# Kernel tuning notes

Measured on AMD Instinct MI355X. Metric: run time of the kernel, lower is better.

The kernel has to match this reference:

```python
import jax, jax.numpy as jnp
import numpy as np

S, B, C, H, M = 384, 8, 1024, 16, 1536
CC = C // H


def setup_inputs() -> dict:
    key = jax.random.key(0)
    ks = jax.random.split(key, 8)
    x = jax.random.normal(ks[0], (S, B, C), dtype=jnp.float32)
    pe = jax.random.normal(ks[1], (S, B, C), dtype=jnp.float32)
    memory_k = jax.random.normal(ks[2], (M, B, H, CC), dtype=jnp.float32)
    memory_v = jax.random.normal(ks[3], (M, B, H, CC), dtype=jnp.float32)
    w_qkv = jax.random.normal(ks[4], (C, 3 * C), dtype=jnp.float32) * 0.02
    b_qkv = jnp.zeros((3 * C,), dtype=jnp.float32)
    w_out = jax.random.normal(ks[5], (C, C), dtype=jnp.float32) * 0.02
    b_out = jnp.zeros((C,), dtype=jnp.float32)
    terminal = jnp.zeros((B,), dtype=bool)
    # causal mask over the new tokens: True = masked (future positions)
    content_mask = jnp.broadcast_to(
        (jnp.arange(S)[None, :] > jnp.arange(S)[:, None])[:, :, None], (S, S, B))
    padding_mask = jnp.zeros((S, B), dtype=bool)  # True = padded
    memory_length = jax.random.randint(ks[6], (B,), 0, M, dtype=jnp.int32)
    return dict(x=x, positional_encoding=pe, memory_k=memory_k, memory_v=memory_v,
                w_qkv=w_qkv, b_qkv=b_qkv, w_out=w_out, b_out=b_out,
                terminal=terminal, content_mask=content_mask,
                padding_mask=padding_mask, memory_length=memory_length)


def reference(x, positional_encoding, memory_k, memory_v, w_qkv, b_qkv,
              w_out, b_out, terminal, content_mask, padding_mask, memory_length):
    s, b, c = x.shape
    # qkv projection
    qkv = (x + positional_encoding) @ w_qkv + b_qkv          # [s,b,3c]
    q, k, v = jnp.split(qkv, 3, axis=-1)
    q = q.reshape(s, b, H, CC)
    k = k.reshape(s, b, H, CC)
    v = v.reshape(s, b, H, CC)
    # clear_memory(terminal): zero lengths for terminal episodes
    mem_len = jnp.where(terminal, 0, memory_length)          # [b]
    # ragged memory concat expressed with fixed capacity M + padding mask
    k_full = jnp.concatenate([memory_k, k], axis=0)          # [M+s,b,H,CC]
    v_full = jnp.concatenate([memory_v, v], axis=0)
    mem_pad = jnp.arange(M)[:, None] >= mem_len[None, :]     # [M,b] True=masked
    kv_pad = jnp.concatenate([mem_pad, padding_mask], axis=0)  # [M+s,b]
    mem_content = jnp.zeros((s, M, b), dtype=bool)           # memory visible to all queries
    full_content = jnp.concatenate([mem_content, content_mask], axis=1)  # [s,M+s,b]
    mask = full_content | kv_pad[None, :, :]                 # [s,M+s,b]
    # attention
    scores = jnp.einsum('sbhc,tbhc->stbh', q, k_full) * (1.0 / np.sqrt(CC))
    scores = jnp.where(mask[:, :, :, None], jnp.float32(-1e9), scores)
    p = jax.nn.softmax(scores, axis=1)                       # [s,M+s,b,h]
    out = jnp.einsum('stbh,tbhc->sbhc', p, v_full).reshape(s, b, c)
    return out @ w_out + b_out
```

## Files before the change

kernel.cpp:

```cpp
#include <hip/hip_runtime.h>
#include <math.h>

#define S_DIM 384
#define B_DIM 8
#define C_DIM 1024
#define H_DIM 16
#define M_DIM 1536
#define CC_DIM 64
#define ROWS  (S_DIM * B_DIM)
#define N3C   (3 * C_DIM)
#define NSPLIT 4

typedef unsigned short u16;
typedef short bf8v  __attribute__((ext_vector_type(8)));
typedef short bf4v  __attribute__((ext_vector_type(4)));
typedef u16   us8   __attribute__((ext_vector_type(8)));
typedef u16   us4   __attribute__((ext_vector_type(4)));
typedef float f4v   __attribute__((ext_vector_type(4)));

__device__ __forceinline__ u16 f2bf(float f) {
    unsigned u = __float_as_uint(f);
    u += 0x7fffu + ((u >> 16) & 1u);
    return (u16)(u >> 16);
}
__device__ __forceinline__ float bf2f(u16 v) {
    return __uint_as_float(((unsigned)v) << 16);
}
#if __has_builtin(__builtin_amdgcn_exp2f)
#define EX2(x) __builtin_amdgcn_exp2f(x)
#else
#define EX2(x) __expf((x) * 0.69314718056f)
#endif
#define QSCALE (0.125f * 1.44269504f)

__device__ __forceinline__ f4v mfma16x16x16bf16(bf4v a, bf4v b, f4v c) {
#if __has_builtin(__builtin_amdgcn_mfma_f32_16x16x16bf16_1k)
    return __builtin_amdgcn_mfma_f32_16x16x16bf16_1k(a, b, c, 0, 0, 0);
#else
    return c;
#endif
}

__device__ __forceinline__ void gload16(const u16* g, u16* l) {
    __builtin_amdgcn_global_load_lds(
        (const __attribute__((address_space(1))) void*)g,
        (__attribute__((address_space(3))) void*)l, 16, 0, 0);
}

__device__ __forceinline__ void tr32(const float* __restrict__ in, u16* __restrict__ out,
                                     int R, int Cc, int r0, int c0, int tid, float* sm) {
    #pragma unroll
    for (int i = 0; i < 4; i++) {
        int r = i * 8 + (tid >> 5), c = tid & 31;
        sm[r * 33 + c] = in[(size_t)(r0 + r) * Cc + c0 + c];
    }
    __syncthreads();
    #pragma unroll
    for (int i = 0; i < 4; i++) {
        int cw = i * 8 + (tid >> 5), rw = tid & 31;
        out[(size_t)(c0 + cw) * R + r0 + rw] = f2bf(sm[rw * 33 + cw]);
    }
}

__global__ __launch_bounds__(256) void prep_all(
    const float* __restrict__ x, const float* __restrict__ pe, u16* __restrict__ Abf,
    const float* __restrict__ wqkv, u16* __restrict__ Wqkvt,
    const float* __restrict__ wout, u16* __restrict__ Woutt,
    const float* __restrict__ mk, u16* __restrict__ mk_bf,
    const float* __restrict__ mv, u16* __restrict__ mv_t)
{
    __shared__ float sm[64 * 65];
    const int bid = blockIdx.x, tid = threadIdx.x;

    if (bid < 3072) {
        size_t i = ((size_t)bid * 256 + tid) * 4;
        float4 xv = *(const float4*)(x + i);
        float4 pv = *(const float4*)(pe + i);
        us4 o;
        o[0] = f2bf(xv.x + pv.x); o[1] = f2bf(xv.y + pv.y);
        o[2] = f2bf(xv.z + pv.z); o[3] = f2bf(xv.w + pv.w);
        *(us4*)(Abf + i) = o;
    } else if (bid < 6144) {
        int b2 = bid - 3072;
        tr32(wqkv, Wqkvt, C_DIM, N3C, (b2 / 96) * 32, (b2 % 96) * 32, tid, sm);
    } else if (bid < 7168) {
        int b3 = bid - 6144;
        tr32(wout, Woutt, C_DIM, C_DIM, (b3 / 32) * 32, (b3 % 32) * 32, tid, sm);
    } else if (bid < 19456) {
        int b4 = bid - 7168;
        size_t i = ((size_t)b4 * 256 + tid) * 4;
        float4 v = *(const float4*)(mk + i);
        us4 o;
        o[0] = f2bf(v.x); o[1] = f2bf(v.y); o[2] = f2bf(v.z); o[3] = f2bf(v.w);
        *(us4*)(mk_bf + i) = o;
    } else {
        int b5 = bid - 19456;
        int bh = b5 & 127;
        int t0 = (b5 >> 7) * 64;
        #pragma unroll
        for (int i = 0; i < 16; i++) {
            int r = i * 4 + (tid >> 6), c = tid & 63;
            sm[r * 65 + c] = mv[((size_t)(t0 + r) * 128 + bh) * 64 + c];
        }
        __syncthreads();
        #pragma unroll
        for (int i = 0; i < 16; i++) {
            int cc = i * 4 + (tid >> 6), tw = tid & 63;
            mv_t[((size_t)bh * 64 + cc) * M_DIM + t0 + tw] = f2bf(sm[tw * 65 + cc]);
        }
    }
}

__global__ __launch_bounds__(256) void prep_vwt(
    const u16* __restrict__ Vw, u16* __restrict__ Vwt)
{
    __shared__ u16 tile[64][66];
    const int tid = threadIdx.x;
    const int bh = blockIdx.x & 127;
    const int t0 = (blockIdx.x >> 7) * 64;
    #pragma unroll
    for (int i = 0; i < 16; i++) {
        int r = i * 4 + (tid >> 6), c = tid & 63;
        tile[r][c] = Vw[((size_t)bh * S_DIM + t0 + r) * 64 + c];
    }
    __syncthreads();
    #pragma unroll
    for (int i = 0; i < 16; i++) {
        int cc = i * 4 + (tid >> 6), tw = tid & 63;
        Vwt[((size_t)bh * 64 + cc) * S_DIM + t0 + tw] = tile[tw][cc];
    }
}

__global__ __launch_bounds__(256) void qkv_gemm(
    const u16* __restrict__ Abf, const u16* __restrict__ Wt,
    const float* __restrict__ bias,
    u16* __restrict__ Qw, u16* __restrict__ Kw, u16* __restrict__ Vw)
{
    __shared__ u16 smem[128 * 64 + 64 * 64];
    u16* As = smem;
    u16* Bs = smem + 128 * 64;
    u16* Cs = smem;

    const int tid = threadIdx.x;
    const int lane = tid & 63, w = tid >> 6;
    const int lr = lane & 15, quad = lane >> 4;
    const int wm = w >> 1, wn = w & 1;
    const int row0 = blockIdx.y * 128, col0 = blockIdx.x * 64;

    f4v acc[4][2];
    #pragma unroll
    for (int i = 0; i < 4; i++)
        #pragma unroll
        for (int j = 0; j < 2; j++)
            acc[i][j] = (f4v){0.f, 0.f, 0.f, 0.f};

    for (int k0 = 0; k0 < C_DIM; k0 += 64) {
        __syncthreads();
        #pragma unroll
        for (int j = 0; j < 4; j++) {
            int idx = j * 256 + tid;
            int r = idx >> 3, c = (idx & 7) ^ (r & 7);
            gload16(&Abf[(size_t)(row0 + r) * C_DIM + k0 + c * 8], &As[idx * 8]);
        }
        #pragma unroll
        for (int j = 0; j < 2; j++) {
            int idx = j * 256 + tid;
            int r = idx >> 3, c = (idx & 7) ^ (r & 7);
            gload16(&Wt[(size_t)(col0 + r) * C_DIM + k0 + c * 8], &Bs[idx * 8]);
        }
        __syncthreads();
        #pragma unroll
        for (int kh = 0; kh < 2; kh++) {
            bf8v a[4], b[2];
            #pragma unroll
            for (int mi = 0; mi < 4; mi++) {
                int row = wm * 64 + mi * 16 + lr;
                int p = (kh * 4 + quad) ^ (lr & 7);
                a[mi] = *(const bf8v*)&As[row * 64 + p * 8];
            }
            #pragma unroll
            for (int nj = 0; nj < 2; nj++) {
                int row = wn * 32 + nj * 16 + lr;
                int p = (kh * 4 + quad) ^ (lr & 7);
                b[nj] = *(const bf8v*)&Bs[row * 64 + p * 8];
            }
            #pragma unroll
            for (int mi = 0; mi < 4; mi++)
                #pragma unroll
                for (int nj = 0; nj < 2; nj++)
                    acc[mi][nj] = __builtin_amdgcn_mfma_f32_16x16x32_bf16(a[mi], b[nj], acc[mi][nj], 0, 0, 0);
        }
    }

    const int which = col0 >> 10;
    const int h = (col0 >> 6) & 15;
    const float qs = (which == 0) ? QSCALE : 1.0f;
    u16* dstbuf = (which == 0) ? Qw : ((which == 1) ? Kw : Vw);

    __syncthreads();
    #pragma unroll
    for (int nj = 0; nj < 2; nj++) {
        int col = col0 + wn * 32 + nj * 16 + lr;
        float bv = bias[col];
        #pragma unroll
        for (int mi = 0; mi < 4; mi++)
            #pragma unroll
            for (int reg = 0; reg < 4; reg++)
                Cs[(wm * 64 + mi * 16 + quad * 4 + reg) * 72 + wn * 32 + nj * 16 + lr] =
                    f2bf((acc[mi][nj][reg] + bv) * qs);
    }
    __syncthreads();
    {
        int r = tid >> 1, half = tid & 1;
        int rg = row0 + r, s = rg >> 3, bb = rg & 7;
        u16* drow = dstbuf + ((size_t)(bb * 16 + h) * S_DIM + s) * 64 + half * 32;
        #pragma unroll
        for (int i = 0; i < 4; i++)
            *(us8*)(drow + i * 8) = *(const us8*)&Cs[r * 72 + half * 32 + i * 8];
    }
}

__global__ __launch_bounds__(256) void attn_split(
    const u16* __restrict__ Qw, const u16* __restrict__ Kw,
    const u16* __restrict__ mk_bf, const u16* __restrict__ Vwt,
    const u16* __restrict__ mv_t, const unsigned char* __restrict__ terminal,
    const int* __restrict__ mem_len, u16* __restrict__ Op, float* __restrict__ ml)
{
    __shared__ u16 smem[2 * 64 * 64];
    u16* Ks = smem;
    u16* Vs = smem + 64 * 64;
    u16* Os = smem;

    const int tid = threadIdx.x;
    const int lane = tid & 63, w = tid >> 6;
    const int lr = lane & 15, quad = lane >> 4, q8 = quad * 8;
    const int bid = blockIdx.x;
    const int split = bid & (NSPLIT - 1);
    const int g = bid / NSPLIT;
    const int b = g & 7, h = (g >> 3) & 15, sc = g >> 7;
    const int bh = b * 16 + h, sq0 = sc * 64;
    const int L = terminal[b] ? 0 : mem_len[b];
    const int qrow = sq0 + w * 16 + lr;

    const u16* qbase = Qw + ((size_t)bh * S_DIM + sq0 + w * 16 + lr) * 64;
    bf8v qf0 = *(const bf8v*)&qbase[q8];
    bf8v qf1 = *(const bf8v*)&qbase[32 + q8];

    f4v O[4];
    #pragma unroll
    for (int nj = 0; nj < 4; nj++) O[nj] = (f4v){0.f, 0.f, 0.f, 0.f};
    float m_i = -1e30f, l_i = 0.0f;

    const int memChunks = (L + 63) >> 6;
    const int total = memChunks + sc + 1;
    const int lo = (split * total) / NSPLIT;
    const int hi = ((split + 1) * total) / NSPLIT;

    const f4v zero = (f4v){0.f, 0.f, 0.f, 0.f};

    for (int ch = lo; ch < hi; ch++) {
        const bool isMem = (ch < memChunks);
        const int tloc = isMem ? ch * 64 : (ch - memChunks) * 64;
        const u16* kb; size_t kstr;
        if (isMem) { kb = mk_bf + ((size_t)tloc * 128 + bh) * 64; kstr = 128 * 64; }
        else       { kb = Kw + ((size_t)bh * S_DIM + tloc) * 64; kstr = 64; }
        const u16* vb; size_t vstr;
        if (isMem) { vb = mv_t + (size_t)bh * 64 * M_DIM + tloc; vstr = M_DIM; }
        else       { vb = Vwt + (size_t)bh * 64 * S_DIM + tloc; vstr = S_DIM; }

        __syncthreads();
        #pragma unroll
        for (int j = 0; j < 2; j++) {
            int idx = j * 256 + tid;
            int r = idx >> 3, c = (idx & 7) ^ (r & 7);
            gload16(kb + (size_t)r * kstr + c * 8, &Ks[idx * 8]);
        }
        #pragma unroll
        for (int j = 0; j < 2; j++) {
            int idx = j * 256 + tid;
            int cc = idx >> 3, c = (idx & 7) ^ (cc & 7);
            gload16(vb + (size_t)cc * vstr + c * 8, &Vs[idx * 8]);
        }
        __syncthreads();

        f4v sv[4];
        #pragma unroll
        for (int tt = 0; tt < 4; tt++) {
            int row = tt * 16 + lr;
            int p0 = quad ^ (lr & 7), p1 = (4 + quad) ^ (lr & 7);
            bf8v k0 = *(const bf8v*)&Ks[row * 64 + p0 * 8];
            bf8v k1 = *(const bf8v*)&Ks[row * 64 + p1 * 8];
            sv[tt] = __builtin_amdgcn_mfma_f32_16x16x32_bf16(k0, qf0, zero, 0, 0, 0);
            sv[tt] = __builtin_amdgcn_mfma_f32_16x16x32_bf16(k1, qf1, sv[tt], 0, 0, 0);
        }

        if (isMem) {
            if (tloc + 64 > L) {
                #pragma unroll
                for (int tt = 0; tt < 4; tt++)
                    #pragma unroll
                    for (int reg = 0; reg < 4; reg++) {
                        int t = tloc + tt * 16 + quad * 4 + reg;
                        if (t >= L) sv[tt][reg] = -1e30f;
                    }
            }
        } else {
            if (tloc + 63 > sq0 + w * 16) {
                #pragma unroll
                for (int tt = 0; tt < 4; tt++)
                    #pragma unroll
                    for (int reg = 0; reg < 4; reg++) {
                        int t = tloc + tt * 16 + quad * 4 + reg;
                        if (t > qrow) sv[tt][reg] = -1e30f;
                    }
            }
        }

        float rowmax = fmaxf(fmaxf(sv[0][0], sv[0][1]), fmaxf(sv[0][2], sv[0][3]));
        #pragma unroll
        for (int tt = 1; tt < 4; tt++)
            rowmax = fmaxf(rowmax, fmaxf(fmaxf(sv[tt][0], sv[tt][1]),
                                         fmaxf(sv[tt][2], sv[tt][3])));
        rowmax = fmaxf(rowmax, __shfl_xor(rowmax, 16));
        rowmax = fmaxf(rowmax, __shfl_xor(rowmax, 32));
        float mnew = fmaxf(m_i, rowmax);
        float alpha = EX2(m_i - mnew);
        m_i = mnew;
        float sum = 0.0f;
        bf4v pf[4];
        #pragma unroll
        for (int tt = 0; tt < 4; tt++) {
            #pragma unroll
            for (int reg = 0; reg < 4; reg++) {
                float p = EX2(sv[tt][reg] - mnew);
                sum += p;
                pf[tt][reg] = (short)f2bf(p);
            }
        }
        sum += __shfl_xor(sum, 16);
        sum += __shfl_xor(sum, 32);
        l_i = l_i * alpha + sum;

        float alphaR[4];
        #pragma unroll
        for (int reg = 0; reg < 4; reg++)
            alphaR[reg] = __shfl(alpha, quad * 4 + reg);
        #pragma unroll
        for (int nj = 0; nj < 4; nj++)
            #pragma unroll
            for (int reg = 0; reg < 4; reg++)
                O[nj][reg] *= alphaR[reg];

        #pragma unroll
        for (int tt = 0; tt < 4; tt++) {
            #pragma unroll
            for (int nj = 0; nj < 4; nj++) {
                int cc = nj * 16 + lr;
                int c = (tt * 2 + (quad >> 1)) ^ (lr & 7);
                bf4v vf = *(const bf4v*)&Vs[cc * 64 + c * 8 + (quad & 1) * 4];
                O[nj] = mfma16x16x16bf16(pf[tt], vf, O[nj]);
            }
        }
    }

    const size_t pbase = (size_t)(g * NSPLIT + split) * 64;
    if (quad == 0) {
        int row = w * 16 + lr;
        float2 mlv = {m_i, l_i};
        *(float2*)&ml[(pbase + row) * 2] = mlv;
    }
    __syncthreads();
    #pragma unroll
    for (int reg = 0; reg < 4; reg++)
        #pragma unroll
        for (int nj = 0; nj < 4; nj++)
            Os[(w * 16 + quad * 4 + reg) * 72 + nj * 16 + lr] = f2bf(O[nj][reg]);
    __syncthreads();
    {
        int row = tid >> 2, q4 = tid & 3;
        us8 v0 = *(const us8*)&Os[row * 72 + q4 * 16];
        us8 v1 = *(const us8*)&Os[row * 72 + q4 * 16 + 8];
        size_t ob = (pbase + row) * 64 + q4 * 16;
        *(us8*)&Op[ob] = v0;
        *(us8*)&Op[ob + 8] = v1;
    }
}

__global__ __launch_bounds__(256) void attn_combine(
    const u16* __restrict__ Op, const float* __restrict__ ml, u16* __restrict__ Obf)
{
    const int g = blockIdx.x;
    const int b = g & 7, h = (g >> 3) & 15, sc = g >> 7;
    const int tid = threadIdx.x;
    const int row = tid >> 2, c0 = (tid & 3) * 16;

    float m[NSPLIT], lv[NSPLIT];
    #pragma unroll
    for (int j = 0; j < NSPLIT; j++) {
        size_t base = (size_t)(g * NSPLIT + j) * 64 + row;
        m[j]  = ml[base * 2];
        lv[j] = ml[base * 2 + 1];
    }
    float mstar = m[0];
    #pragma unroll
    for (int j = 1; j < NSPLIT; j++) mstar = fmaxf(mstar, m[j]);
    float sc_j[NSPLIT], l = 0.0f;
    #pragma unroll
    for (int j = 0; j < NSPLIT; j++) {
        sc_j[j] = EX2(m[j] - mstar);
        l += sc_j[j] * lv[j];
    }
    float inv = 1.0f / l;

    float o[16];
    #pragma unroll
    for (int c = 0; c < 16; c++) o[c] = 0.0f;
    #pragma unroll
    for (int j = 0; j < NSPLIT; j++) {
        const u16* src = &Op[((size_t)(g * NSPLIT + j) * 64 + row) * 64 + c0];
        us8 v0 = *(const us8*)src;
        us8 v1 = *(const us8*)(src + 8);
        #pragma unroll
        for (int c = 0; c < 8; c++) {
            o[c]     += sc_j[j] * bf2f(v0[c]);
            o[c + 8] += sc_j[j] * bf2f(v1[c]);
        }
    }
    int s = sc * 64 + row;
    size_t dst = ((size_t)s * 8 + b) * C_DIM + h * 64 + c0;
    us8 w0, w1;
    #pragma unroll
    for (int c = 0; c < 8; c++) {
        w0[c] = f2bf(o[c] * inv);
        w1[c] = f2bf(o[c + 8] * inv);
    }
    *(us8*)&Obf[dst] = w0;
    *(us8*)&Obf[dst + 8] = w1;
}

__global__ __launch_bounds__(256) void proj_gemm(
    const u16* __restrict__ Abf, const u16* __restrict__ Wt,
    const float* __restrict__ bias, float* __restrict__ out)
{
    __shared__ u16 As[128 * 64];
    __shared__ u16 Bs[64 * 64];
    const int tid = threadIdx.x;
    const int lane = tid & 63, w = tid >> 6;
    const int lr = lane & 15, quad = lane >> 4;
    const int wm = w >> 1, wn = w & 1;
    const int row0 = blockIdx.y * 128, col0 = blockIdx.x * 64;

    f4v acc[4][2];
    #pragma unroll
    for (int i = 0; i < 4; i++)
        #pragma unroll
        for (int j = 0; j < 2; j++)
            acc[i][j] = (f4v){0.f, 0.f, 0.f, 0.f};

    for (int k0 = 0; k0 < C_DIM; k0 += 64) {
        __syncthreads();
        #pragma unroll
        for (int j = 0; j < 4; j++) {
            int idx = j * 256 + tid;
            int r = idx >> 3, c = (idx & 7) ^ (r & 7);
            gload16(&Abf[(size_t)(row0 + r) * C_DIM + k0 + c * 8], &As[idx * 8]);
        }
        #pragma unroll
        for (int j = 0; j < 2; j++) {
            int idx = j * 256 + tid;
            int r = idx >> 3, c = (idx & 7) ^ (r & 7);
            gload16(&Wt[(size_t)(col0 + r) * C_DIM + k0 + c * 8], &Bs[idx * 8]);
        }
        __syncthreads();
        #pragma unroll
        for (int kh = 0; kh < 2; kh++) {
            bf8v a[4], b[2];
            #pragma unroll
            for (int mi = 0; mi < 4; mi++) {
                int row = wm * 64 + mi * 16 + lr;
                int p = (kh * 4 + quad) ^ (lr & 7);
                a[mi] = *(const bf8v*)&As[row * 64 + p * 8];
            }
            #pragma unroll
            for (int nj = 0; nj < 2; nj++) {
                int row = wn * 32 + nj * 16 + lr;
                int p = (kh * 4 + quad) ^ (lr & 7);
                b[nj] = *(const bf8v*)&Bs[row * 64 + p * 8];
            }
            #pragma unroll
            for (int mi = 0; mi < 4; mi++)
                #pragma unroll
                for (int nj = 0; nj < 2; nj++)
                    acc[mi][nj] = __builtin_amdgcn_mfma_f32_16x16x32_bf16(a[mi], b[nj], acc[mi][nj], 0, 0, 0);
        }
    }

    #pragma unroll
    for (int nj = 0; nj < 2; nj++) {
        int col = col0 + wn * 32 + nj * 16 + lr;
        float bv = bias[col];
        #pragma unroll
        for (int mi = 0; mi < 4; mi++) {
            #pragma unroll
            for (int reg = 0; reg < 4; reg++) {
                int rg = row0 + wm * 64 + mi * 16 + quad * 4 + reg;
                out[(size_t)rg * C_DIM + col] = acc[mi][nj][reg] + bv;
            }
        }
    }
}

extern "C" void kernel_launch(void* const* d_in, const int* in_sizes, int n_in,
                              void* d_out, int out_size, void* d_ws, size_t ws_size,
                              hipStream_t stream) {
    const float* x    = (const float*)d_in[0];
    const float* pe   = (const float*)d_in[1];
    const float* mk   = (const float*)d_in[2];
    const float* mv   = (const float*)d_in[3];
    const float* wqkv = (const float*)d_in[4];
    const float* bqkv = (const float*)d_in[5];
    const float* wout = (const float*)d_in[6];
    const float* bout = (const float*)d_in[7];
    const unsigned char* term = (const unsigned char*)d_in[8];
    const int* mem_len = (const int*)d_in[11];

    char* ws = (char*)d_ws;
    u16* Abf   = (u16*)(ws + 0);
    u16* Obf   = (u16*)(ws + 0);
    u16* Wqkvt = (u16*)(ws + 6291456);
    u16* Vwt   = (u16*)(ws + 6291456);
    u16* Woutt = (u16*)(ws + 12582912);
    u16* mk_bf = (u16*)(ws + 14680064);
    u16* mv_t  = (u16*)(ws + 39845888);
    u16* Qw    = (u16*)(ws + 65011712);
    u16* Kw    = (u16*)(ws + 71303168);
    u16* Vw    = (u16*)(ws + 77594624);
    u16* Op    = (u16*)(ws + 83886080);
    float* ml  = (float*)(ws + 109051904);

    float* out = (float*)d_out;

    prep_all<<<22528, 256, 0, stream>>>(x, pe, Abf, wqkv, Wqkvt, wout, Woutt,
                                        mk, mk_bf, mv, mv_t);

    qkv_gemm<<<dim3(N3C / 64, ROWS / 128), 256, 0, stream>>>(
        Abf, Wqkvt, bqkv, Qw, Kw, Vw);

    prep_vwt<<<(S_DIM / 64) * 128, 256, 0, stream>>>(Vw, Vwt);

    attn_split<<<B_DIM * H_DIM * (S_DIM / 64) * NSPLIT, 256, 0, stream>>>(
        Qw, Kw, mk_bf, Vwt, mv_t, term, mem_len, Op, ml);

    attn_combine<<<B_DIM * H_DIM * (S_DIM / 64), 256, 0, stream>>>(Op, ml, Obf);

    proj_gemm<<<dim3(C_DIM / 64, ROWS / 128), 256, 0, stream>>>(
        Obf, Woutt, bout, out);
}
```

Before: 303.2 us.

## Fuse V transpose into QKV GEMM, fixed-size attention splits, smaller proj tiles

Several changes land together. The QKV GEMM epilogue now writes V already transposed, so the separate prep_vwt kernel and its launch are removed. Attention splits the KV range into fixed 6-chunk pieces, up to 5 splits per query tile; blocks with no work exit early and the combine step reads only the splits that exist. The projection GEMM moves to 64x64 tiles for more blocks, the prep kernel handles two vectors per thread, and the attention output is written straight from registers instead of staged through LDS. The trade-offs are uncoalesced scalar Op stores and more partial buffers than before.

```diff
diff --git a/kernel.cpp b/kernel.cpp
--- a/kernel.cpp
+++ b/kernel.cpp
@@ -9,7 +9,8 @@
 #define CC_DIM 64
 #define ROWS  (S_DIM * B_DIM)
 #define N3C   (3 * C_DIM)
-#define NSPLIT 4
+#define CHUNK 6
+#define MAXS  5
 
 typedef unsigned short u16;
 typedef short bf8v  __attribute__((ext_vector_type(8)));
@@ -72,29 +73,36 @@
     __shared__ float sm[64 * 65];
     const int bid = blockIdx.x, tid = threadIdx.x;
 
-    if (bid < 3072) {
-        size_t i = ((size_t)bid * 256 + tid) * 4;
-        float4 xv = *(const float4*)(x + i);
-        float4 pv = *(const float4*)(pe + i);
-        us4 o;
-        o[0] = f2bf(xv.x + pv.x); o[1] = f2bf(xv.y + pv.y);
-        o[2] = f2bf(xv.z + pv.z); o[3] = f2bf(xv.w + pv.w);
-        *(us4*)(Abf + i) = o;
-    } else if (bid < 6144) {
-        int b2 = bid - 3072;
+    if (bid < 1536) {
+        size_t i0 = (size_t)bid * 2048 + tid * 4;
+        #pragma unroll
+        for (int j = 0; j < 2; j++) {
+            size_t i = i0 + j * 1024;
+            float4 xv = *(const float4*)(x + i);
+            float4 pv = *(const float4*)(pe + i);
+            us4 o;
+            o[0] = f2bf(xv.x + pv.x); o[1] = f2bf(xv.y + pv.y);
+            o[2] = f2bf(xv.z + pv.z); o[3] = f2bf(xv.w + pv.w);
+            *(us4*)(Abf + i) = o;
+        }
+    } else if (bid < 4608) {
+        int b2 = bid - 1536;
         tr32(wqkv, Wqkvt, C_DIM, N3C, (b2 / 96) * 32, (b2 % 96) * 32, tid, sm);
-    } else if (bid < 7168) {
-        int b3 = bid - 6144;
+    } else if (bid < 5632) {
+        int b3 = bid - 4608;
         tr32(wout, Woutt, C_DIM, C_DIM, (b3 / 32) * 32, (b3 % 32) * 32, tid, sm);
-    } else if (bid < 19456) {
-        int b4 = bid - 7168;
-        size_t i = ((size_t)b4 * 256 + tid) * 4;
-        float4 v = *(const float4*)(mk + i);
-        us4 o;
-        o[0] = f2bf(v.x); o[1] = f2bf(v.y); o[2] = f2bf(v.z); o[3] = f2bf(v.w);
-        *(us4*)(mk_bf + i) = o;
+    } else if (bid < 11776) {
+        size_t i0 = (size_t)(bid - 5632) * 2048 + tid * 4;
+        #pragma unroll
+        for (int j = 0; j < 2; j++) {
+            size_t i = i0 + j * 1024;
+            float4 v = *(const float4*)(mk + i);
+            us4 o;
+            o[0] = f2bf(v.x); o[1] = f2bf(v.y); o[2] = f2bf(v.z); o[3] = f2bf(v.w);
+            *(us4*)(mk_bf + i) = o;
+        }
     } else {
-        int b5 = bid - 19456;
+        int b5 = bid - 11776;
         int bh = b5 & 127;
         int t0 = (b5 >> 7) * 64;
         #pragma unroll
@@ -111,30 +119,10 @@
     }
 }
 
-__global__ __launch_bounds__(256) void prep_vwt(
-    const u16* __restrict__ Vw, u16* __restrict__ Vwt)
-{
-    __shared__ u16 tile[64][66];
-    const int tid = threadIdx.x;
-    const int bh = blockIdx.x & 127;
-    const int t0 = (blockIdx.x >> 7) * 64;
-    #pragma unroll
-    for (int i = 0; i < 16; i++) {
-        int r = i * 4 + (tid >> 6), c = tid & 63;
-        tile[r][c] = Vw[((size_t)bh * S_DIM + t0 + r) * 64 + c];
-    }
-    __syncthreads();
-    #pragma unroll
-    for (int i = 0; i < 16; i++) {
-        int cc = i * 4 + (tid >> 6), tw = tid & 63;
-        Vwt[((size_t)bh * 64 + cc) * S_DIM + t0 + tw] = tile[tw][cc];
-    }
-}
-
 __global__ __launch_bounds__(256) void qkv_gemm(
     const u16* __restrict__ Abf, const u16* __restrict__ Wt,
     const float* __restrict__ bias,
-    u16* __restrict__ Qw, u16* __restrict__ Kw, u16* __restrict__ Vw)
+    u16* __restrict__ Qw, u16* __restrict__ Kw, u16* __restrict__ Vwt)
 {
     __shared__ u16 smem[128 * 64 + 64 * 64];
     u16* As = smem;
@@ -195,7 +183,6 @@
     const int which = col0 >> 10;
     const int h = (col0 >> 6) & 15;
     const float qs = (which == 0) ? QSCALE : 1.0f;
-    u16* dstbuf = (which == 0) ? Qw : ((which == 1) ? Kw : Vw);
 
     __syncthreads();
     #pragma unroll
@@ -210,13 +197,31 @@
                     f2bf((acc[mi][nj][reg] + bv) * qs);
     }
     __syncthreads();
-    {
+
+    if (which != 2) {
+        u16* dstbuf = (which == 0) ? Qw : Kw;
         int r = tid >> 1, half = tid & 1;
         int rg = row0 + r, s = rg >> 3, bb = rg & 7;
         u16* drow = dstbuf + ((size_t)(bb * 16 + h) * S_DIM + s) * 64 + half * 32;
         #pragma unroll
         for (int i = 0; i < 4; i++)
             *(us8*)(drow + i * 8) = *(const us8*)&Cs[r * 72 + half * 32 + i * 8];
+    } else {
+        int cc = tid & 63, w4 = tid >> 6;
+        int s0 = row0 >> 3;
+        #pragma unroll
+        for (int pb = 0; pb < 2; pb++) {
+            int bb = w4 * 2 + pb;
+            us8 v0, v1;
+            #pragma unroll
+            for (int sl = 0; sl < 8; sl++) {
+                v0[sl] = Cs[(sl * 8 + bb) * 72 + cc];
+                v1[sl] = Cs[((sl + 8) * 8 + bb) * 72 + cc];
+            }
+            u16* dr = Vwt + ((size_t)(bb * 16 + h) * 64 + cc) * S_DIM + s0;
+            *(us8*)dr = v0;
+            *(us8*)(dr + 8) = v1;
+        }
     }
 }
 
@@ -226,20 +231,24 @@
     const u16* __restrict__ mv_t, const unsigned char* __restrict__ terminal,
     const int* __restrict__ mem_len, u16* __restrict__ Op, float* __restrict__ ml)
 {
-    __shared__ u16 smem[2 * 64 * 64];
-    u16* Ks = smem;
-    u16* Vs = smem + 64 * 64;
-    u16* Os = smem;
+    __shared__ u16 Ks[64 * 64];
+    __shared__ u16 Vs[64 * 64];
 
     const int tid = threadIdx.x;
     const int lane = tid & 63, w = tid >> 6;
     const int lr = lane & 15, quad = lane >> 4, q8 = quad * 8;
     const int bid = blockIdx.x;
-    const int split = bid & (NSPLIT - 1);
-    const int g = bid / NSPLIT;
+    const int j = bid % MAXS;
+    const int g = bid / MAXS;
     const int b = g & 7, h = (g >> 3) & 15, sc = g >> 7;
     const int bh = b * 16 + h, sq0 = sc * 64;
     const int L = terminal[b] ? 0 : mem_len[b];
+    const int memChunks = (L + 63) >> 6;
+    const int total = memChunks + sc + 1;
+    const int lo = j * CHUNK;
+    const int hi = (lo + CHUNK < total) ? lo + CHUNK : total;
+    if (lo >= total) return;
+
     const int qrow = sq0 + w * 16 + lr;
 
     const u16* qbase = Qw + ((size_t)bh * S_DIM + sq0 + w * 16 + lr) * 64;
@@ -250,11 +259,6 @@
     #pragma unroll
     for (int nj = 0; nj < 4; nj++) O[nj] = (f4v){0.f, 0.f, 0.f, 0.f};
     float m_i = -1e30f, l_i = 0.0f;
-
-    const int memChunks = (L + 63) >> 6;
-    const int total = memChunks + sc + 1;
-    const int lo = (split * total) / NSPLIT;
-    const int hi = ((split + 1) * total) / NSPLIT;
 
     const f4v zero = (f4v){0.f, 0.f, 0.f, 0.f};
 
@@ -270,14 +274,14 @@
 
         __syncthreads();
         #pragma unroll
-        for (int j = 0; j < 2; j++) {
-            int idx = j * 256 + tid;
+        for (int jj = 0; jj < 2; jj++) {
+            int idx = jj * 256 + tid;
             int r = idx >> 3, c = (idx & 7) ^ (r & 7);
             gload16(kb + (size_t)r * kstr + c * 8, &Ks[idx * 8]);
         }
         #pragma unroll
-        for (int j = 0; j < 2; j++) {
-            int idx = j * 256 + tid;
+        for (int jj = 0; jj < 2; jj++) {
+            int idx = jj * 256 + tid;
             int cc = idx >> 3, c = (idx & 7) ^ (cc & 7);
             gload16(vb + (size_t)cc * vstr + c * 8, &Vs[idx * 8]);
         }
@@ -363,30 +367,23 @@
         }
     }
 
-    const size_t pbase = (size_t)(g * NSPLIT + split) * 64;
+    const size_t pbase = (size_t)(g * MAXS + j) * 64;
     if (quad == 0) {
         int row = w * 16 + lr;
         float2 mlv = {m_i, l_i};
         *(float2*)&ml[(pbase + row) * 2] = mlv;
     }
-    __syncthreads();
-    #pragma unroll
-    for (int reg = 0; reg < 4; reg++)
+    #pragma unroll
+    for (int reg = 0; reg < 4; reg++) {
+        int row = w * 16 + quad * 4 + reg;
         #pragma unroll
         for (int nj = 0; nj < 4; nj++)
-            Os[(w * 16 + quad * 4 + reg) * 72 + nj * 16 + lr] = f2bf(O[nj][reg]);
-    __syncthreads();
-    {
-        int row = tid >> 2, q4 = tid & 3;
-        us8 v0 = *(const us8*)&Os[row * 72 + q4 * 16];
-        us8 v1 = *(const us8*)&Os[row * 72 + q4 * 16 + 8];
-        size_t ob = (pbase + row) * 64 + q4 * 16;
-        *(us8*)&Op[ob] = v0;
-        *(us8*)&Op[ob + 8] = v1;
+            Op[(pbase + row) * 64 + nj * 16 + lr] = f2bf(O[nj][reg]);
     }
 }
 
 __global__ __launch_bounds__(256) void attn_combine(
+    const unsigned char* __restrict__ terminal, const int* __restrict__ mem_len,
     const u16* __restrict__ Op, const float* __restrict__ ml, u16* __restrict__ Obf)
 {
     const int g = blockIdx.x;
@@ -394,20 +391,26 @@
     const int tid = threadIdx.x;
     const int row = tid >> 2, c0 = (tid & 3) * 16;
 
-    float m[NSPLIT], lv[NSPLIT];
-    #pragma unroll
-    for (int j = 0; j < NSPLIT; j++) {
-        size_t base = (size_t)(g * NSPLIT + j) * 64 + row;
-        m[j]  = ml[base * 2];
-        lv[j] = ml[base * 2 + 1];
+    const int L = terminal[b] ? 0 : mem_len[b];
+    const int total = ((L + 63) >> 6) + sc + 1;
+    const int nsp = (total + CHUNK - 1) / CHUNK;
+
+    float m[MAXS], lv[MAXS];
+    #pragma unroll
+    for (int j = 0; j < MAXS; j++) {
+        if (j < nsp) {
+            size_t base = (size_t)(g * MAXS + j) * 64 + row;
+            m[j]  = ml[base * 2];
+            lv[j] = ml[base * 2 + 1];
+        } else { m[j] = -1e30f; lv[j] = 0.0f; }
     }
     float mstar = m[0];
     #pragma unroll
-    for (int j = 1; j < NSPLIT; j++) mstar = fmaxf(mstar, m[j]);
-    float sc_j[NSPLIT], l = 0.0f;
-    #pragma unroll
-    for (int j = 0; j < NSPLIT; j++) {
-        sc_j[j] = EX2(m[j] - mstar);
+    for (int j = 1; j < MAXS; j++) mstar = fmaxf(mstar, m[j]);
+    float sc_j[MAXS], l = 0.0f;
+    #pragma unroll
+    for (int j = 0; j < MAXS; j++) {
+        sc_j[j] = (j < nsp) ? EX2(m[j] - mstar) : 0.0f;
         l += sc_j[j] * lv[j];
     }
     float inv = 1.0f / l;
@@ -415,9 +418,8 @@
     float o[16];
     #pragma unroll
     for (int c = 0; c < 16; c++) o[c] = 0.0f;
-    #pragma unroll
-    for (int j = 0; j < NSPLIT; j++) {
-        const u16* src = &Op[((size_t)(g * NSPLIT + j) * 64 + row) * 64 + c0];
+    for (int j = 0; j < nsp; j++) {
+        const u16* src = &Op[((size_t)(g * MAXS + j) * 64 + row) * 64 + c0];
         us8 v0 = *(const us8*)src;
         us8 v1 = *(const us8*)(src + 8);
         #pragma unroll
@@ -442,70 +444,47 @@
     const u16* __restrict__ Abf, const u16* __restrict__ Wt,
     const float* __restrict__ bias, float* __restrict__ out)
 {
-    __shared__ u16 As[128 * 64];
+    __shared__ u16 As[64 * 64];
     __shared__ u16 Bs[64 * 64];
     const int tid = threadIdx.x;
     const int lane = tid & 63, w = tid >> 6;
     const int lr = lane & 15, quad = lane >> 4;
-    const int wm = w >> 1, wn = w & 1;
-    const int row0 = blockIdx.y * 128, col0 = blockIdx.x * 64;
-
-    f4v acc[4][2];
-    #pragma unroll
-    for (int i = 0; i < 4; i++)
-        #pragma unroll
-        for (int j = 0; j < 2; j++)
-            acc[i][j] = (f4v){0.f, 0.f, 0.f, 0.f};
+    const int row0 = blockIdx.y * 64, col0 = blockIdx.x * 64;
+
+    f4v acc[4];
+    #pragma unroll
+    for (int i = 0; i < 4; i++) acc[i] = (f4v){0.f, 0.f, 0.f, 0.f};
 
     for (int k0 = 0; k0 < C_DIM; k0 += 64) {
         __syncthreads();
         #pragma unroll
-        for (int j = 0; j < 4; j++) {
+        for (int j = 0; j < 2; j++) {
             int idx = j * 256 + tid;
             int r = idx >> 3, c = (idx & 7) ^ (r & 7);
             gload16(&Abf[(size_t)(row0 + r) * C_DIM + k0 + c * 8], &As[idx * 8]);
-        }
-        #pragma unroll
-        for (int j = 0; j < 2; j++) {
-            int idx = j * 256 + tid;
-            int r = idx >> 3, c = (idx & 7) ^ (r & 7);
             gload16(&Wt[(size_t)(col0 + r) * C_DIM + k0 + c * 8], &Bs[idx * 8]);
         }
         __syncthreads();
         #pragma unroll
         for (int kh = 0; kh < 2; kh++) {
-            bf8v a[4], b[2];
-            #pragma unroll
-            for (int mi = 0; mi < 4; mi++) {
-                int row = wm * 64 + mi * 16 + lr;
-                int p = (kh * 4 + quad) ^ (lr & 7);
-                a[mi] = *(const bf8v*)&As[row * 64 + p * 8];
-            }
-            #pragma unroll
-            for (int nj = 0; nj < 2; nj++) {
-                int row = wn * 32 + nj * 16 + lr;
-                int p = (kh * 4 + quad) ^ (lr & 7);
-                b[nj] = *(const bf8v*)&Bs[row * 64 + p * 8];
-            }
-            #pragma unroll
-            for (int mi = 0; mi < 4; mi++)
-                #pragma unroll
-                for (int nj = 0; nj < 2; nj++)
-                    acc[mi][nj] = __builtin_amdgcn_mfma_f32_16x16x32_bf16(a[mi], b[nj], acc[mi][nj], 0, 0, 0);
-        }
-    }
-
-    #pragma unroll
-    for (int nj = 0; nj < 2; nj++) {
-        int col = col0 + wn * 32 + nj * 16 + lr;
+            int p = (kh * 4 + quad) ^ (lr & 7);
+            bf8v a = *(const bf8v*)&As[(w * 16 + lr) * 64 + p * 8];
+            #pragma unroll
+            for (int nj = 0; nj < 4; nj++) {
+                bf8v bfr = *(const bf8v*)&Bs[(nj * 16 + lr) * 64 + p * 8];
+                acc[nj] = __builtin_amdgcn_mfma_f32_16x16x32_bf16(a, bfr, acc[nj], 0, 0, 0);
+            }
+        }
+    }
+
+    #pragma unroll
+    for (int nj = 0; nj < 4; nj++) {
+        int col = col0 + nj * 16 + lr;
         float bv = bias[col];
         #pragma unroll
-        for (int mi = 0; mi < 4; mi++) {
-            #pragma unroll
-            for (int reg = 0; reg < 4; reg++) {
-                int rg = row0 + wm * 64 + mi * 16 + quad * 4 + reg;
-                out[(size_t)rg * C_DIM + col] = acc[mi][nj][reg] + bv;
-            }
+        for (int reg = 0; reg < 4; reg++) {
+            int rg = row0 + w * 16 + quad * 4 + reg;
+            out[(size_t)rg * C_DIM + col] = acc[nj][reg] + bv;
         }
     }
 }
@@ -528,31 +507,29 @@
     u16* Abf   = (u16*)(ws + 0);
     u16* Obf   = (u16*)(ws + 0);
     u16* Wqkvt = (u16*)(ws + 6291456);
-    u16* Vwt   = (u16*)(ws + 6291456);
+    float* ml  = (float*)(ws + 6291456);
     u16* Woutt = (u16*)(ws + 12582912);
     u16* mk_bf = (u16*)(ws + 14680064);
     u16* mv_t  = (u16*)(ws + 39845888);
     u16* Qw    = (u16*)(ws + 65011712);
     u16* Kw    = (u16*)(ws + 71303168);
-    u16* Vw    = (u16*)(ws + 77594624);
+    u16* Vwt   = (u16*)(ws + 77594624);
     u16* Op    = (u16*)(ws + 83886080);
-    float* ml  = (float*)(ws + 109051904);
 
     float* out = (float*)d_out;
 
-    prep_all<<<22528, 256, 0, stream>>>(x, pe, Abf, wqkv, Wqkvt, wout, Woutt,
+    prep_all<<<14848, 256, 0, stream>>>(x, pe, Abf, wqkv, Wqkvt, wout, Woutt,
                                         mk, mk_bf, mv, mv_t);
 
     qkv_gemm<<<dim3(N3C / 64, ROWS / 128), 256, 0, stream>>>(
-        Abf, Wqkvt, bqkv, Qw, Kw, Vw);
-
-    prep_vwt<<<(S_DIM / 64) * 128, 256, 0, stream>>>(Vw, Vwt);
-
-    attn_split<<<B_DIM * H_DIM * (S_DIM / 64) * NSPLIT, 256, 0, stream>>>(
+        Abf, Wqkvt, bqkv, Qw, Kw, Vwt);
+
+    attn_split<<<B_DIM * H_DIM * (S_DIM / 64) * MAXS, 256, 0, stream>>>(
         Qw, Kw, mk_bf, Vwt, mv_t, term, mem_len, Op, ml);
 
-    attn_combine<<<B_DIM * H_DIM * (S_DIM / 64), 256, 0, stream>>>(Op, ml, Obf);
-
-    proj_gemm<<<dim3(C_DIM / 64, ROWS / 128), 256, 0, stream>>>(
+    attn_combine<<<B_DIM * H_DIM * (S_DIM / 64), 256, 0, stream>>>(
+        term, mem_len, Op, ml, Obf);
+
+    proj_gemm<<<dim3(C_DIM / 64, ROWS / 64), 256, 0, stream>>>(
         Obf, Woutt, bout, out);
 }
```

Measured after the change: 287.2 us. 1.06x faster.
